# Optimization experiments

Hardware: AMD Instinct MI355X
Metric: run time of the kernel (lower is better)

Reference implementation:

```python
import jax, jax.numpy as jnp
import numpy as np

VOCAB, EMBED, HID = 30000, 256, 128
B, T = 256, 512


def setup_inputs() -> dict:
    key = jax.random.key(0)
    ks = jax.random.split(key, 8)
    s_e = 1.0 / np.sqrt(EMBED)
    s_h = 1.0 / np.sqrt(HID)
    return {
        "tokens": jax.random.randint(ks[0], (B, T), 0, VOCAB, dtype=jnp.int32),
        "emb": jax.random.uniform(ks[1], (VOCAB, EMBED), jnp.float32, -0.05, 0.05),
        "W_fw": jax.random.normal(ks[2], (EMBED, 4 * HID), jnp.float32) * s_e,
        "U_fw": jax.random.normal(ks[3], (HID, 4 * HID), jnp.float32) * s_h,
        "b_fw": jnp.zeros((4 * HID,), jnp.float32),
        "W_bw": jax.random.normal(ks[4], (EMBED, 4 * HID), jnp.float32) * s_e,
        "U_bw": jax.random.normal(ks[5], (HID, 4 * HID), jnp.float32) * s_h,
        "b_bw": jnp.zeros((4 * HID,), jnp.float32),
    }


def _lstm_scan(x, W, U, b):
    # x: [B, T, E]; Keras LSTMCell gate order i, f, g(c), o.
    xW = jnp.einsum("bte,eg->btg", x, W) + b  # precompute input projections

    def step(carry, xw_t):
        h, c = carry
        z = xw_t + h @ U  # [B, 4H]
        i, f, g, o = jnp.split(z, 4, axis=-1)
        c = jax.nn.sigmoid(f) * c + jax.nn.sigmoid(i) * jnp.tanh(g)
        h = jax.nn.sigmoid(o) * jnp.tanh(c)
        return (h, c), h

    h0 = jnp.zeros((x.shape[0], U.shape[0]), x.dtype)
    (h_T, c_T), hs = jax.lax.scan(step, (h0, h0), xW.transpose(1, 0, 2))
    return hs.transpose(1, 0, 2), h_T, c_T  # [B,T,H], [B,H], [B,H]


def reference(tokens, emb, W_fw, U_fw, b_fw, W_bw, U_bw, b_bw):
    x = emb[tokens]  # [B, T, E]; Dropout layers are identity in eval mode
    out_f, hf, cf = _lstm_scan(x, W_fw, U_fw, b_fw)
    out_b_rev, hb, cb = _lstm_scan(x[:, ::-1, :], W_bw, U_bw, b_bw)
    out = jnp.concatenate([out_f, out_b_rev[:, ::-1, :]], axis=-1)  # [B,T,2H]
    return out, hf, cf, hb, cb
```

## Files before the change

### kernel.cpp

```cpp
#include <hip/hip_runtime.h>
#include <hip/hip_bf16.h>
#include <stdint.h>

#define VOCAB 30000
#define EMBED 256
#define HID   128
#define BB    256
#define TT    512
#define G4    512
#define GWH   1024

typedef _Float16 f16x8 __attribute__((ext_vector_type(8)));
typedef _Float16 f16x4 __attribute__((ext_vector_type(4)));
typedef float    f32x4 __attribute__((ext_vector_type(4)));

#define S_IFO (-1.4426950408889634f)
#define S_G   ( 2.8853900817779268f)

__device__ __forceinline__ float fexp2(float x){
#if __has_builtin(__builtin_amdgcn_exp2f)
  return __builtin_amdgcn_exp2f(x);
#else
  return exp2f(x);
#endif
}
__device__ __forceinline__ float frcp(float x){
#if __has_builtin(__builtin_amdgcn_rcpf)
  return __builtin_amdgcn_rcpf(x);
#else
  return 1.0f/x;
#endif
}
__device__ __forceinline__ float sigm_p(float zp){
  return frcp(1.0f + fexp2(zp));
}
__device__ __forceinline__ float tanh_p(float zp){
  return 1.0f - 2.0f*frcp(1.0f + fexp2(zp));
}
__device__ __forceinline__ float tanh_rt(float x){
  return 1.0f - 2.0f*frcp(1.0f + fexp2(S_G*x));
}

__global__ __launch_bounds__(256, 4) void embw_mfma(
    const float* __restrict__ emb,
    const float* __restrict__ Wf, const float* __restrict__ Wb,
    const float* __restrict__ bf, const float* __restrict__ bb,
    _Float16* __restrict__ EW)
{
  __shared__ _Float16 As[64*EMBED];
  const int tid  = threadIdx.x;
  const int l    = tid & 63;
  const int w    = tid >> 6;
  const int r0   = blockIdx.x * 64;
  const int dirc = blockIdx.y >> 3;
  const int u0   = (blockIdx.y & 7) * 16;
  const int nr   = min(64, VOCAB - r0);

  const float4* asrc = (const float4*)(emb + (size_t)r0*EMBED);
  for (int i = tid; i < nr*(EMBED/4); i += 256){
    float4 v = asrc[i];
    const int row = i >> 6;
    const int kc  = (i & 63) * 4;
    const int ks  = kc ^ ((row & 7) << 3);
    _Float16* dst = &As[row*EMBED + ks];
    dst[0]=(_Float16)v.x; dst[1]=(_Float16)v.y;
    dst[2]=(_Float16)v.z; dst[3]=(_Float16)v.w;
  }
  __syncthreads();

  const int cl = w*16 + (l & 15);
  const int ul = cl >> 2;
  const int g  = cl & 3;
  const int cg = g*128 + u0 + ul;
  const float* Wsrc = (dirc ? Wb : Wf) + cg;
  const int kg = (l >> 4) * 8;

  f32x4 acc[4] = {{0,0,0,0},{0,0,0,0},{0,0,0,0},{0,0,0,0}};

  for (int kk = 0; kk < EMBED/32; ++kk){
    const int kb = kk*32 + kg;
    f16x8 bfrag;
    #pragma unroll
    for (int j = 0; j < 8; ++j)
      bfrag[j] = (_Float16)Wsrc[(size_t)(kb + j)*G4];
    #pragma unroll
    for (int m = 0; m < 4; ++m){
      const int row = m*16 + (l & 15);
      const int ks  = kb ^ ((row & 7) << 3);
      f16x8 afrag = *(const f16x8*)&As[row*EMBED + ks];
      acc[m] = __builtin_amdgcn_mfma_f32_16x16x32_f16(afrag, bfrag, acc[m], 0, 0, 0);
    }
  }

  const float bv  = (dirc ? bb : bf)[cg];
  const float gsc = (g == 2) ? S_G : S_IFO;
  const int   co  = dirc*512 + (u0 + ul)*4 + g;
  #pragma unroll
  for (int m = 0; m < 4; ++m){
    #pragma unroll
    for (int r = 0; r < 4; ++r){
      const int vrow = r0 + m*16 + (l >> 4)*4 + r;
      if (vrow < VOCAB)
        EW[(size_t)vrow*GWH + co] = (_Float16)((acc[m][r] + bv) * gsc);
    }
  }
}

__global__ __launch_bounds__(512, 2) void lstm_r10(
    const int*      __restrict__ tokens,
    const _Float16* __restrict__ EW,
    const float*    __restrict__ Ufw, const float* __restrict__ Ubw,
    float* __restrict__ out)
{
  __shared__ _Float16 h_lds[2][320];
  __shared__ int      tok_lds[2*TT];

  const int tid = threadIdx.x;
  const int l   = tid & 63;
  const int w   = tid >> 6;
  const int lr  = l & 15;
  const int hi  = l >> 4;
  const int dir = blockIdx.x & 1;
  const int b0  = (blockIdx.x >> 1) * 2;

  if (tid < 640) ((_Float16*)h_lds)[tid] = (_Float16)0.f;
  for (int i = tid; i < 2*TT; i += 512)
    tok_lds[i] = tokens[(b0 + (i >> 9))*TT + (i & 511)];
  __syncthreads();

  const float* U = dir ? Ubw : Ufw;
  f16x8 ub[4][4];
  #pragma unroll
  for (int kt = 0; kt < 4; ++kt){
    #pragma unroll
    for (int g = 0; g < 4; ++g){
      const int   col = g*128 + w*16 + lr;
      const float gs  = (g == 2) ? S_G : S_IFO;
      f16x8 f;
      #pragma unroll
      for (int j = 0; j < 8; ++j)
        f[j] = (_Float16)(U[(size_t)(kt*32 + hi*8 + j)*G4 + col] * gs);
      ub[kt][g] = f;
    }
  }

  const int  bsel = (l >> 2) & 1;
  const bool act  = (l < 32);
  const int  q    = hi & 1;
  const int  u    = w*16 + lr;

  float creg = 0.f, hfin = 0.f;
  const _Float16* ebase = EW + dir*512 + u*4;

  f32x4 aP[4];
  #pragma unroll
  for (int g = 0; g < 4; ++g) aP[g] = (f32x4){0.f,0.f,0.f,0.f};

  #define AADDR(S) ({ int ss_ = (S); ss_ = ss_ < TT ? ss_ : TT-1;            \
                      const int tt_ = dir ? (TT-1-ss_) : ss_;                \
                      ebase + (size_t)tok_lds[q*TT + tt_]*GWH; })

  f16x4 xwA = *(const f16x4*)AADDR(0);
  f16x4 xwB = *(const f16x4*)AADDR(1);
  const _Float16* adA = AADDR(2);
  const _Float16* adB = AADDR(3);

  #define STEP(XW, AD, SCUR, CUR)                                            \
  {                                                                          \
    const int t_ = dir ? (TT-1-(SCUR)) : (SCUR);                             \
    f16x8 ha[4];                                                             \
    _Pragma("unroll")                                                        \
    for (int kt = 0; kt < 4; ++kt)                                           \
      ha[kt] = *(const f16x8*)&h_lds[CUR][bsel*160 + kt*32 + hi*8];          \
    _Pragma("unroll")                                                        \
    for (int g = 0; g < 4; ++g) aP[g][0] = (float)XW[g];                     \
    XW = *(const f16x4*)AD;                 \
    AD = AADDR((SCUR)+4);                   \
    _Pragma("unroll")                                                        \
    for (int kt = 0; kt < 4; ++kt){                                          \
      _Pragma("unroll")                                                      \
      for (int g = 0; g < 4; ++g)                                            \
        aP[g] = __builtin_amdgcn_mfma_f32_16x16x32_f16(ha[kt], ub[kt][g], aP[g], 0,0,0); \
    }                                                                        \
    if (act){                                                                \
      const float si = sigm_p(aP[0][0]);                                     \
      const float sf = sigm_p(aP[1][0]);                                     \
      const float tg = tanh_p(aP[2][0]);                                     \
      const float so = sigm_p(aP[3][0]);                                     \
      const float cn = sf*creg + si*tg;                                      \
      creg = cn;                                                             \
      const float hh = so*tanh_rt(cn);                                       \
      hfin = hh;                                                             \
      h_lds[(CUR)^1][q*160 + u] = (_Float16)hh;                              \
      out[((size_t)(b0+q)*TT + t_)*(2*HID) + (size_t)dir*HID + u] = hh;      \
    }                                                                        \
    asm volatile("s_waitcnt lgkmcnt(0)" ::: "memory");                       \
    __builtin_amdgcn_s_barrier();                                            \
  }

  for (int s = 0; s < TT; s += 2){
    STEP(xwA, adA, s,     0)
    STEP(xwB, adB, s + 1, 1)
  }
  #undef STEP
  #undef AADDR

  if (act){
    const size_t O1  = (size_t)BB*TT*(2*HID);
    const size_t idx = (size_t)(b0+q)*HID + u;
    if (dir == 0){
      out[O1                    + idx] = hfin;
      out[O1 +   (size_t)BB*HID + idx] = creg;
    } else {
      out[O1 + 2*(size_t)BB*HID + idx] = hfin;
      out[O1 + 3*(size_t)BB*HID + idx] = creg;
    }
  }
}

extern "C" void kernel_launch(void* const* d_in, const int* in_sizes, int n_in,
                              void* d_out, int out_size, void* d_ws, size_t ws_size,
                              hipStream_t stream)
{
  const int*   tokens = (const int*)  d_in[0];
  const float* emb    = (const float*)d_in[1];
  const float* Wf     = (const float*)d_in[2];
  const float* Ufw    = (const float*)d_in[3];
  const float* bf     = (const float*)d_in[4];
  const float* Wb     = (const float*)d_in[5];
  const float* Ubw    = (const float*)d_in[6];
  const float* bb     = (const float*)d_in[7];
  float* out = (float*)d_out;
  _Float16* EW = (_Float16*)d_ws;

  embw_mfma<<<dim3((VOCAB + 63)/64, 16), 256, 0, stream>>>(emb, Wf, Wb, bf, bb, EW);
  lstm_r10<<<BB, 512, 0, stream>>>(tokens, EW, Ufw, Ubw, out);
}
```

Baseline: 370.6 us.

## Split recurrent MFMA chain into two accumulators and read tokens from global

The serial per-step chain of 16 dependent MFMAs is split into two independent accumulator sets (aP over k-tiles 0 and 1, aQ over k-tiles 2 and 3), interleaved and summed before the activations. This shortens the dependent MFMA latency on the recurrence's critical path. The token LDS staging is also removed: active lanes now read token ids straight from global memory one step ahead, and the gate-row gather is predicated on active lanes only. The cost is extra accumulator registers and a small global load per step on the prefetch path.

```diff
diff --git a/kernel.cpp b/kernel.cpp
--- a/kernel.cpp
+++ b/kernel.cpp
@@ -106,14 +106,13 @@
   }
 }
 
-__global__ __launch_bounds__(512, 2) void lstm_r10(
+__global__ __launch_bounds__(512, 2) void lstm_r11(
     const int*      __restrict__ tokens,
     const _Float16* __restrict__ EW,
     const float*    __restrict__ Ufw, const float* __restrict__ Ubw,
     float* __restrict__ out)
 {
   __shared__ _Float16 h_lds[2][320];
-  __shared__ int      tok_lds[2*TT];
 
   const int tid = threadIdx.x;
   const int l   = tid & 63;
@@ -124,8 +123,6 @@
   const int b0  = (blockIdx.x >> 1) * 2;
 
   if (tid < 640) ((_Float16*)h_lds)[tid] = (_Float16)0.f;
-  for (int i = tid; i < 2*TT; i += 512)
-    tok_lds[i] = tokens[(b0 + (i >> 9))*TT + (i & 511)];
   __syncthreads();
 
   const float* U = dir ? Ubw : Ufw;
@@ -151,21 +148,25 @@
 
   float creg = 0.f, hfin = 0.f;
   const _Float16* ebase = EW + dir*512 + u*4;
-
-  f32x4 aP[4];
+  const int* tokq = tokens + (size_t)(b0+q)*TT;
+
+  #define TIDX(S) ({ int ss_ = (S); ss_ = ss_ < TT ? ss_ : TT-1;             \
+                     dir ? (TT-1-ss_) : ss_; })
+
+  f32x4 aP[4], aQ[4];
   #pragma unroll
-  for (int g = 0; g < 4; ++g) aP[g] = (f32x4){0.f,0.f,0.f,0.f};
-
-  #define AADDR(S) ({ int ss_ = (S); ss_ = ss_ < TT ? ss_ : TT-1;            \
-                      const int tt_ = dir ? (TT-1-ss_) : ss_;                \
-                      ebase + (size_t)tok_lds[q*TT + tt_]*GWH; })
-
-  f16x4 xwA = *(const f16x4*)AADDR(0);
-  f16x4 xwB = *(const f16x4*)AADDR(1);
-  const _Float16* adA = AADDR(2);
-  const _Float16* adB = AADDR(3);
-
-  #define STEP(XW, AD, SCUR, CUR)                                            \
+  for (int g = 0; g < 4; ++g){ aP[g]=(f32x4){0,0,0,0}; aQ[g]=(f32x4){0,0,0,0}; }
+
+  int tkA = 0, tkB = 0;
+  f16x4 xwA = {0,0,0,0}, xwB = {0,0,0,0};
+  if (act){
+    xwA = *(const f16x4*)(ebase + (size_t)tokq[TIDX(0)]*GWH);
+    xwB = *(const f16x4*)(ebase + (size_t)tokq[TIDX(1)]*GWH);
+    tkA = tokq[TIDX(2)];
+    tkB = tokq[TIDX(3)];
+  }
+
+  #define STEP(XW, TK, SCUR, CUR)                                            \
   {                                                                          \
     const int t_ = dir ? (TT-1-(SCUR)) : (SCUR);                             \
     f16x8 ha[4];                                                             \
@@ -173,20 +174,29 @@
     for (int kt = 0; kt < 4; ++kt)                                           \
       ha[kt] = *(const f16x8*)&h_lds[CUR][bsel*160 + kt*32 + hi*8];          \
     _Pragma("unroll")                                                        \
-    for (int g = 0; g < 4; ++g) aP[g][0] = (float)XW[g];                     \
-    XW = *(const f16x4*)AD;                 \
-    AD = AADDR((SCUR)+4);                   \
-    _Pragma("unroll")                                                        \
-    for (int kt = 0; kt < 4; ++kt){                                          \
-      _Pragma("unroll")                                                      \
-      for (int g = 0; g < 4; ++g)                                            \
-        aP[g] = __builtin_amdgcn_mfma_f32_16x16x32_f16(ha[kt], ub[kt][g], aP[g], 0,0,0); \
+    for (int g = 0; g < 4; ++g){ aP[g][0] = (float)XW[g]; aQ[g][0] = 0.f; }  \
+    if (act){                                                                \
+      const _Float16* ad_ = ebase + (size_t)TK*GWH;  \
+      XW = *(const f16x4*)ad_;                        \
+      TK = tokq[TIDX((SCUR)+4)];                      \
     }                                                                        \
+    _Pragma("unroll")                                                        \
+    for (int g = 0; g < 4; ++g)                                              \
+      aP[g] = __builtin_amdgcn_mfma_f32_16x16x32_f16(ha[0], ub[0][g], aP[g], 0,0,0); \
+    _Pragma("unroll")                                                        \
+    for (int g = 0; g < 4; ++g)                                              \
+      aQ[g] = __builtin_amdgcn_mfma_f32_16x16x32_f16(ha[2], ub[2][g], aQ[g], 0,0,0); \
+    _Pragma("unroll")                                                        \
+    for (int g = 0; g < 4; ++g)                                              \
+      aP[g] = __builtin_amdgcn_mfma_f32_16x16x32_f16(ha[1], ub[1][g], aP[g], 0,0,0); \
+    _Pragma("unroll")                                                        \
+    for (int g = 0; g < 4; ++g)                                              \
+      aQ[g] = __builtin_amdgcn_mfma_f32_16x16x32_f16(ha[3], ub[3][g], aQ[g], 0,0,0); \
     if (act){                                                                \
-      const float si = sigm_p(aP[0][0]);                                     \
-      const float sf = sigm_p(aP[1][0]);                                     \
-      const float tg = tanh_p(aP[2][0]);                                     \
-      const float so = sigm_p(aP[3][0]);                                     \
+      const float si = sigm_p(aP[0][0] + aQ[0][0]);                          \
+      const float sf = sigm_p(aP[1][0] + aQ[1][0]);                          \
+      const float tg = tanh_p(aP[2][0] + aQ[2][0]);                          \
+      const float so = sigm_p(aP[3][0] + aQ[3][0]);                          \
       const float cn = sf*creg + si*tg;                                      \
       creg = cn;                                                             \
       const float hh = so*tanh_rt(cn);                                       \
@@ -199,11 +209,11 @@
   }
 
   for (int s = 0; s < TT; s += 2){
-    STEP(xwA, adA, s,     0)
-    STEP(xwB, adB, s + 1, 1)
+    STEP(xwA, tkA, s,     0)
+    STEP(xwB, tkB, s + 1, 1)
   }
   #undef STEP
-  #undef AADDR
+  #undef TIDX
 
   if (act){
     const size_t O1  = (size_t)BB*TT*(2*HID);
@@ -234,5 +244,5 @@
   _Float16* EW = (_Float16*)d_ws;
 
   embw_mfma<<<dim3((VOCAB + 63)/64, 16), 256, 0, stream>>>(emb, Wf, Wb, bf, bb, EW);
-  lstm_r10<<<BB, 512, 0, stream>>>(tokens, EW, Ufw, Ubw, out);
-}
+  lstm_r11<<<BB, 512, 0, stream>>>(tokens, EW, Ufw, Ubw, out);
+}
```

Result: slower. 389.5 us (+5.1%).

## Interleave forward and backward LSTM directions in one block per batch row

Applied to the files above, without the earlier changes.

Each block now handles a single batch row and runs both directions, alternating phases so the gate activations of one direction overlap the MFMA recurrence of the other. Before, each block handled two batch rows of a single direction. The aim is to hide the serial latency between the MFMA and the gate math within each timestep. In exchange, register pressure doubles because both directions' U fragments are held in registers, and only 16 lanes per wave do gate work.

```diff
diff --git a/kernel.cpp b/kernel.cpp
--- a/kernel.cpp
+++ b/kernel.cpp
@@ -31,15 +31,9 @@
   return 1.0f/x;
 #endif
 }
-__device__ __forceinline__ float sigm_p(float zp){
-  return frcp(1.0f + fexp2(zp));
-}
-__device__ __forceinline__ float tanh_p(float zp){
-  return 1.0f - 2.0f*frcp(1.0f + fexp2(zp));
-}
-__device__ __forceinline__ float tanh_rt(float x){
-  return 1.0f - 2.0f*frcp(1.0f + fexp2(S_G*x));
-}
+__device__ __forceinline__ float sigm_p(float zp){ return frcp(1.0f + fexp2(zp)); }
+__device__ __forceinline__ float tanh_p(float zp){ return 1.0f - 2.0f*frcp(1.0f + fexp2(zp)); }
+__device__ __forceinline__ float tanh_rt(float x){ return 1.0f - 2.0f*frcp(1.0f + fexp2(S_G*x)); }
 
 __global__ __launch_bounds__(256, 4) void embw_mfma(
     const float* __restrict__ emb,
@@ -106,115 +100,140 @@
   }
 }
 
-__global__ __launch_bounds__(512, 2) void lstm_r10(
+__global__ __launch_bounds__(512, 2) void lstm_dp(
     const int*      __restrict__ tokens,
     const _Float16* __restrict__ EW,
     const float*    __restrict__ Ufw, const float* __restrict__ Ubw,
     float* __restrict__ out)
 {
-  __shared__ _Float16 h_lds[2][320];
-  __shared__ int      tok_lds[2*TT];
+  __shared__ _Float16 h_lds[2][160];
+  __shared__ int      tok_lds[TT];
 
   const int tid = threadIdx.x;
   const int l   = tid & 63;
   const int w   = tid >> 6;
   const int lr  = l & 15;
   const int hi  = l >> 4;
-  const int dir = blockIdx.x & 1;
-  const int b0  = (blockIdx.x >> 1) * 2;
-
-  if (tid < 640) ((_Float16*)h_lds)[tid] = (_Float16)0.f;
-  for (int i = tid; i < 2*TT; i += 512)
-    tok_lds[i] = tokens[(b0 + (i >> 9))*TT + (i & 511)];
+  const int b   = blockIdx.x;
+
+  if (tid < 320) ((_Float16*)h_lds)[tid] = (_Float16)0.f;
+  if (tid < TT)  tok_lds[tid] = tokens[(size_t)b*TT + tid];
   __syncthreads();
 
-  const float* U = dir ? Ubw : Ufw;
-  f16x8 ub[4][4];
+  f16x8 ub[2][4][4];
   #pragma unroll
-  for (int kt = 0; kt < 4; ++kt){
-    #pragma unroll
-    for (int g = 0; g < 4; ++g){
-      const int   col = g*128 + w*16 + lr;
-      const float gs  = (g == 2) ? S_G : S_IFO;
-      f16x8 f;
+  for (int d = 0; d < 2; ++d){
+    const float* U = d ? Ubw : Ufw;
+    #pragma unroll
+    for (int kt = 0; kt < 4; ++kt){
       #pragma unroll
-      for (int j = 0; j < 8; ++j)
-        f[j] = (_Float16)(U[(size_t)(kt*32 + hi*8 + j)*G4 + col] * gs);
-      ub[kt][g] = f;
-    }
-  }
-
-  const int  bsel = (l >> 2) & 1;
-  const bool act  = (l < 32);
-  const int  q    = hi & 1;
-  const int  u    = w*16 + lr;
-
-  float creg = 0.f, hfin = 0.f;
-  const _Float16* ebase = EW + dir*512 + u*4;
-
-  f32x4 aP[4];
+      for (int g = 0; g < 4; ++g){
+        const int   col = g*128 + w*16 + lr;
+        const float gs  = (g == 2) ? S_G : S_IFO;
+        f16x8 f;
+        #pragma unroll
+        for (int j = 0; j < 8; ++j)
+          f[j] = (_Float16)(U[(size_t)(kt*32 + hi*8 + j)*G4 + col] * gs);
+        ub[d][kt][g] = f;
+      }
+    }
+  }
+
+  const bool act = (l < 16);
+  const int  u   = w*16 + lr;
+
+  float cF = 0.f, cB = 0.f, hFv = 0.f, hBv = 0.f;
+  const _Float16* eb0 = EW +       u*4;
+  const _Float16* eb1 = EW + 512 + u*4;
+
+  #define ADDR_F(S) (eb0 + (size_t)tok_lds[(S) < TT ? (S) : TT-1]*GWH)
+  #define ADDR_B(S) (eb1 + (size_t)tok_lds[(S) < TT ? TT-1-(S) : 0]*GWH)
+
+  f32x4 aF[4], aB[4];
   #pragma unroll
-  for (int g = 0; g < 4; ++g) aP[g] = (f32x4){0.f,0.f,0.f,0.f};
-
-  #define AADDR(S) ({ int ss_ = (S); ss_ = ss_ < TT ? ss_ : TT-1;            \
-                      const int tt_ = dir ? (TT-1-ss_) : ss_;                \
-                      ebase + (size_t)tok_lds[q*TT + tt_]*GWH; })
-
-  f16x4 xwA = *(const f16x4*)AADDR(0);
-  f16x4 xwB = *(const f16x4*)AADDR(1);
-  const _Float16* adA = AADDR(2);
-  const _Float16* adB = AADDR(3);
-
-  #define STEP(XW, AD, SCUR, CUR)                                            \
-  {                                                                          \
-    const int t_ = dir ? (TT-1-(SCUR)) : (SCUR);                             \
-    f16x8 ha[4];                                                             \
+  for (int g = 0; g < 4; ++g){ aF[g]=(f32x4){0,0,0,0}; aB[g]=(f32x4){0,0,0,0}; }
+
+  f16x4 xwF = {0,0,0,0}, xwB = {0,0,0,0};
+  const _Float16 *adF = eb0, *adB = eb1;
+  if (act){
+    xwF = *(const f16x4*)ADDR_F(0);
+    xwB = *(const f16x4*)ADDR_B(0);
+    adF = ADDR_F(1);
+    adB = ADDR_B(1);
+    #pragma unroll
+    for (int g = 0; g < 4; ++g){ aF[g][0] = (float)xwF[g]; aB[g][0] = (float)xwB[g]; }
+    xwF = *(const f16x4*)adF;  adF = ADDR_F(2);
+    xwB = *(const f16x4*)adB;  adB = ADDR_B(2);
+  }
+
+  #define MFMA_PH(ACC, D)                                                    \
+  { f16x8 ha[4];                                                             \
     _Pragma("unroll")                                                        \
     for (int kt = 0; kt < 4; ++kt)                                           \
-      ha[kt] = *(const f16x8*)&h_lds[CUR][bsel*160 + kt*32 + hi*8];          \
-    _Pragma("unroll")                                                        \
-    for (int g = 0; g < 4; ++g) aP[g][0] = (float)XW[g];                     \
-    XW = *(const f16x4*)AD;                 \
-    AD = AADDR((SCUR)+4);                   \
+      ha[kt] = *(const f16x8*)&h_lds[D][kt*32 + hi*8];                       \
     _Pragma("unroll")                                                        \
     for (int kt = 0; kt < 4; ++kt){                                          \
       _Pragma("unroll")                                                      \
       for (int g = 0; g < 4; ++g)                                            \
-        aP[g] = __builtin_amdgcn_mfma_f32_16x16x32_f16(ha[kt], ub[kt][g], aP[g], 0,0,0); \
-    }                                                                        \
-    if (act){                                                                \
-      const float si = sigm_p(aP[0][0]);                                     \
-      const float sf = sigm_p(aP[1][0]);                                     \
-      const float tg = tanh_p(aP[2][0]);                                     \
-      const float so = sigm_p(aP[3][0]);                                     \
-      const float cn = sf*creg + si*tg;                                      \
-      creg = cn;                                                             \
-      const float hh = so*tanh_rt(cn);                                       \
-      hfin = hh;                                                             \
-      h_lds[(CUR)^1][q*160 + u] = (_Float16)hh;                              \
-      out[((size_t)(b0+q)*TT + t_)*(2*HID) + (size_t)dir*HID + u] = hh;      \
-    }                                                                        \
-    asm volatile("s_waitcnt lgkmcnt(0)" ::: "memory");                       \
-    __builtin_amdgcn_s_barrier();                                            \
-  }
-
-  for (int s = 0; s < TT; s += 2){
-    STEP(xwA, adA, s,     0)
-    STEP(xwB, adB, s + 1, 1)
-  }
-  #undef STEP
-  #undef AADDR
+        ACC[g] = __builtin_amdgcn_mfma_f32_16x16x32_f16(ha[kt], ub[D][kt][g], ACC[g], 0,0,0); \
+    } }
+
+  #define GATE_PH(ACC, XW, AD, ADDR_M, CREG, HFIN, SNEXT, T_, DIRC)          \
+  if (act){                                                                  \
+    const float si = sigm_p(ACC[0][0]);                                      \
+    const float sf = sigm_p(ACC[1][0]);                                      \
+    const float tg = tanh_p(ACC[2][0]);                                      \
+    const float so = sigm_p(ACC[3][0]);                                      \
+    const float cn = sf*CREG + si*tg;                                        \
+    CREG = cn;                                                               \
+    const float hh = so*tanh_rt(cn);                                         \
+    HFIN = hh;                                                               \
+    h_lds[DIRC][u] = (_Float16)hh;                                           \
+    out[((size_t)b*TT + (T_))*(2*HID) + (size_t)(DIRC)*HID + u] = hh;        \
+    _Pragma("unroll")                                                        \
+    for (int g = 0; g < 4; ++g) ACC[g][0] = (float)XW[g];                    \
+    XW = *(const f16x4*)AD;                                                  \
+    AD = ADDR_M(SNEXT);                                                      \
+  }
+
+  for (int i = 0; i < TT; ++i){
+    if (i > 0){
+      GATE_PH(aB, xwB, adB, ADDR_B, cB, hBv, i+2, (TT-1-(i-1)), 1)
+    }
+    MFMA_PH(aF, 0)
+    asm volatile("s_waitcnt lgkmcnt(0)" ::: "memory");
+    __builtin_amdgcn_s_barrier();
+
+    GATE_PH(aF, xwF, adF, ADDR_F, cF, hFv, i+3, i, 0)
+    MFMA_PH(aB, 1)
+    asm volatile("s_waitcnt lgkmcnt(0)" ::: "memory");
+    __builtin_amdgcn_s_barrier();
+  }
+
+  if (act){
+    const float si = sigm_p(aB[0][0]);
+    const float sf = sigm_p(aB[1][0]);
+    const float tg = tanh_p(aB[2][0]);
+    const float so = sigm_p(aB[3][0]);
+    const float cn = sf*cB + si*tg;
+    cB = cn;
+    const float hh = so*tanh_rt(cn);
+    hBv = hh;
+    out[((size_t)b*TT + 0)*(2*HID) + HID + u] = hh;
+  }
+
+  #undef GATE_PH
+  #undef MFMA_PH
+  #undef ADDR_F
+  #undef ADDR_B
 
   if (act){
     const size_t O1  = (size_t)BB*TT*(2*HID);
-    const size_t idx = (size_t)(b0+q)*HID + u;
-    if (dir == 0){
-      out[O1                    + idx] = hfin;
-      out[O1 +   (size_t)BB*HID + idx] = creg;
-    } else {
-      out[O1 + 2*(size_t)BB*HID + idx] = hfin;
-      out[O1 + 3*(size_t)BB*HID + idx] = creg;
-    }
+    const size_t idx = (size_t)b*HID + u;
+    out[O1                        + idx] = hFv;
+    out[O1 +   (size_t)BB*HID     + idx] = cF;
+    out[O1 + 2*(size_t)BB*HID     + idx] = hBv;
+    out[O1 + 3*(size_t)BB*HID     + idx] = cB;
   }
 }
 
@@ -234,5 +253,5 @@
   _Float16* EW = (_Float16*)d_ws;
 
   embw_mfma<<<dim3((VOCAB + 63)/64, 16), 256, 0, stream>>>(emb, Wf, Wb, bf, bb, EW);
-  lstm_r10<<<BB, 512, 0, stream>>>(tokens, EW, Ufw, Ubw, out);
-}
+  lstm_dp<<<BB, 512, 0, stream>>>(tokens, EW, Ufw, Ubw, out);
+}
```

Result: slower. 574.5 us (+55.0%).

## Process 16 batch rows per LSTM block to fill MFMA rows

Applied to the files above, without the earlier changes.

Each recurrent block now handles 16 batch sequences instead of 2, so all 16 rows of each MFMA tile carry real work and every lane runs the gate activations for 4 rows. The hidden state in LDS becomes a 16x128 tile with an XOR swizzle to avoid bank conflicts. The input projections now enter as the MFMA accumulator seed rather than being written into a zeroed accumulator. The grid shrinks from 256 to 32 blocks, which leaves most compute units idle while each block does 8x the per-step work on a serial time loop.

```diff
diff --git a/kernel.cpp b/kernel.cpp
--- a/kernel.cpp
+++ b/kernel.cpp
@@ -9,6 +9,7 @@
 #define TT    512
 #define G4    512
 #define GWH   1024
+#define BPB   16
 
 typedef _Float16 f16x8 __attribute__((ext_vector_type(8)));
 typedef _Float16 f16x4 __attribute__((ext_vector_type(4)));
@@ -31,15 +32,9 @@
   return 1.0f/x;
 #endif
 }
-__device__ __forceinline__ float sigm_p(float zp){
-  return frcp(1.0f + fexp2(zp));
-}
-__device__ __forceinline__ float tanh_p(float zp){
-  return 1.0f - 2.0f*frcp(1.0f + fexp2(zp));
-}
-__device__ __forceinline__ float tanh_rt(float x){
-  return 1.0f - 2.0f*frcp(1.0f + fexp2(S_G*x));
-}
+__device__ __forceinline__ float sigm_p(float zp){ return frcp(1.0f + fexp2(zp)); }
+__device__ __forceinline__ float tanh_p(float zp){ return 1.0f - 2.0f*frcp(1.0f + fexp2(zp)); }
+__device__ __forceinline__ float tanh_rt(float x){ return 1.0f - 2.0f*frcp(1.0f + fexp2(S_G*x)); }
 
 __global__ __launch_bounds__(256, 4) void embw_mfma(
     const float* __restrict__ emb,
@@ -106,14 +101,14 @@
   }
 }
 
-__global__ __launch_bounds__(512, 2) void lstm_r10(
+__global__ __launch_bounds__(512, 2) void lstm_b16(
     const int*      __restrict__ tokens,
     const _Float16* __restrict__ EW,
     const float*    __restrict__ Ufw, const float* __restrict__ Ubw,
     float* __restrict__ out)
 {
-  __shared__ _Float16 h_lds[2][320];
-  __shared__ int      tok_lds[2*TT];
+  __shared__ _Float16 h_lds[2][16*HID];
+  __shared__ int      tok_lds[BPB*TT];
 
   const int tid = threadIdx.x;
   const int l   = tid & 63;
@@ -121,10 +116,10 @@
   const int lr  = l & 15;
   const int hi  = l >> 4;
   const int dir = blockIdx.x & 1;
-  const int b0  = (blockIdx.x >> 1) * 2;
-
-  if (tid < 640) ((_Float16*)h_lds)[tid] = (_Float16)0.f;
-  for (int i = tid; i < 2*TT; i += 512)
+  const int b0  = (blockIdx.x >> 1) * BPB;
+
+  for (int i = tid; i < 2*16*HID; i += 512) ((_Float16*)h_lds)[i] = (_Float16)0.f;
+  for (int i = tid; i < BPB*TT; i += 512)
     tok_lds[i] = tokens[(b0 + (i >> 9))*TT + (i & 511)];
   __syncthreads();
 
@@ -144,76 +139,108 @@
     }
   }
 
-  const int  bsel = (l >> 2) & 1;
-  const bool act  = (l < 32);
-  const int  q    = hi & 1;
-  const int  u    = w*16 + lr;
-
-  float creg = 0.f, hfin = 0.f;
+  const int u = w*16 + lr;
+  f32x4 creg = {0.f,0.f,0.f,0.f};
+  float hfin[4] = {0.f,0.f,0.f,0.f};
   const _Float16* ebase = EW + dir*512 + u*4;
-
-  f32x4 aP[4];
+  float* outp[4];
   #pragma unroll
-  for (int g = 0; g < 4; ++g) aP[g] = (f32x4){0.f,0.f,0.f,0.f};
-
-  #define AADDR(S) ({ int ss_ = (S); ss_ = ss_ < TT ? ss_ : TT-1;            \
-                      const int tt_ = dir ? (TT-1-ss_) : ss_;                \
-                      ebase + (size_t)tok_lds[q*TT + tt_]*GWH; })
-
-  f16x4 xwA = *(const f16x4*)AADDR(0);
-  f16x4 xwB = *(const f16x4*)AADDR(1);
-  const _Float16* adA = AADDR(2);
-  const _Float16* adB = AADDR(3);
-
-  #define STEP(XW, AD, SCUR, CUR)                                            \
+  for (int r = 0; r < 4; ++r)
+    outp[r] = out + (size_t)(b0 + hi*4 + r)*TT*(2*HID) + (size_t)dir*HID + u;
+
+  #define TIDX(S) ({ int ss_ = (S); ss_ = ss_ < TT ? ss_ : TT-1;             \
+                     dir ? (TT-1-ss_) : ss_; })
+
+  f16x4 ldA[4], ldB[4];
+  const _Float16 *adA[4], *adB[4];
+  {
+    const int t0 = TIDX(0), t1 = TIDX(1), t2 = TIDX(2), t3 = TIDX(3);
+    #pragma unroll
+    for (int r = 0; r < 4; ++r){
+      ldA[r] = *(const f16x4*)(ebase + (size_t)tok_lds[(hi*4+r)*TT + t0]*GWH);
+      ldB[r] = *(const f16x4*)(ebase + (size_t)tok_lds[(hi*4+r)*TT + t1]*GWH);
+      adA[r] = ebase + (size_t)tok_lds[(hi*4+r)*TT + t2]*GWH;
+      adB[r] = ebase + (size_t)tok_lds[(hi*4+r)*TT + t3]*GWH;
+    }
+  }
+
+  #define STEP(LD, AD, SCUR, CUR)                                            \
   {                                                                          \
     const int t_ = dir ? (TT-1-(SCUR)) : (SCUR);                             \
+         \
     f16x8 ha[4];                                                             \
     _Pragma("unroll")                                                        \
-    for (int kt = 0; kt < 4; ++kt)                                           \
-      ha[kt] = *(const f16x8*)&h_lds[CUR][bsel*160 + kt*32 + hi*8];          \
-    _Pragma("unroll")                                                        \
-    for (int g = 0; g < 4; ++g) aP[g][0] = (float)XW[g];                     \
-    XW = *(const f16x4*)AD;                 \
-    AD = AADDR((SCUR)+4);                   \
-    _Pragma("unroll")                                                        \
     for (int kt = 0; kt < 4; ++kt){                                          \
+      const int chunk = (kt*4 + hi) ^ (lr & 7);                              \
+      ha[kt] = *(const f16x8*)&h_lds[CUR][lr*HID + chunk*8];                 \
+    }                                                                        \
+    int tk4[4];                                                              \
+    { const int t4 = TIDX((SCUR)+4);                                         \
+      _Pragma("unroll")                                                      \
+      for (int r = 0; r < 4; ++r) tk4[r] = tok_lds[(hi*4+r)*TT + t4]; }      \
+                                         \
+    f32x4 cin[4];                                                            \
+    _Pragma("unroll")                                                        \
+    for (int g = 0; g < 4; ++g){                                             \
+      _Pragma("unroll")                                                      \
+      for (int r = 0; r < 4; ++r) cin[g][r] = (float)LD[r][g];               \
+    }                                                                        \
+        \
+    _Pragma("unroll")                                                        \
+    for (int r = 0; r < 4; ++r){                                             \
+      LD[r] = *(const f16x4*)AD[r];                                          \
+      AD[r] = ebase + (size_t)tk4[r]*GWH;                                    \
+    }                                                                        \
+                      \
+    f32x4 acc[4];                                                            \
+    _Pragma("unroll")                                                        \
+    for (int g = 0; g < 4; ++g)                                              \
+      acc[g] = __builtin_amdgcn_mfma_f32_16x16x32_f16(ha[0], ub[0][g], cin[g], 0,0,0); \
+    _Pragma("unroll")                                                        \
+    for (int kt = 1; kt < 4; ++kt){                                          \
       _Pragma("unroll")                                                      \
       for (int g = 0; g < 4; ++g)                                            \
-        aP[g] = __builtin_amdgcn_mfma_f32_16x16x32_f16(ha[kt], ub[kt][g], aP[g], 0,0,0); \
-    }                                                                        \
-    if (act){                                                                \
-      const float si = sigm_p(aP[0][0]);                                     \
-      const float sf = sigm_p(aP[1][0]);                                     \
-      const float tg = tanh_p(aP[2][0]);                                     \
-      const float so = sigm_p(aP[3][0]);                                     \
-      const float cn = sf*creg + si*tg;                                      \
-      creg = cn;                                                             \
+        acc[g] = __builtin_amdgcn_mfma_f32_16x16x32_f16(ha[kt], ub[kt][g], acc[g], 0,0,0); \
+    }                                                                        \
+                         \
+    _Pragma("unroll")                                                        \
+    for (int r = 0; r < 4; ++r){                                             \
+      const float si = sigm_p(acc[0][r]);                                    \
+      const float sf = sigm_p(acc[1][r]);                                    \
+      const float tg = tanh_p(acc[2][r]);                                    \
+      const float so = sigm_p(acc[3][r]);                                    \
+      const float cn = sf*creg[r] + si*tg;                                   \
+      creg[r] = cn;                                                          \
       const float hh = so*tanh_rt(cn);                                       \
-      hfin = hh;                                                             \
-      h_lds[(CUR)^1][q*160 + u] = (_Float16)hh;                              \
-      out[((size_t)(b0+q)*TT + t_)*(2*HID) + (size_t)dir*HID + u] = hh;      \
+      hfin[r] = hh;                                                          \
+      const int row  = hi*4 + r;                                             \
+      const int fidx = row*HID + ((((u >> 3) ^ (row & 7)) & 15) << 3) + (u & 7); \
+      h_lds[(CUR)^1][fidx] = (_Float16)hh;                                   \
+      outp[r][(size_t)t_*(2*HID)] = hh;                                      \
     }                                                                        \
     asm volatile("s_waitcnt lgkmcnt(0)" ::: "memory");                       \
     __builtin_amdgcn_s_barrier();                                            \
   }
 
   for (int s = 0; s < TT; s += 2){
-    STEP(xwA, adA, s,     0)
-    STEP(xwB, adB, s + 1, 1)
+    STEP(ldA, adA, s,     0)
+    STEP(ldB, adB, s + 1, 1)
   }
   #undef STEP
-  #undef AADDR
-
-  if (act){
-    const size_t O1  = (size_t)BB*TT*(2*HID);
-    const size_t idx = (size_t)(b0+q)*HID + u;
-    if (dir == 0){
-      out[O1                    + idx] = hfin;
-      out[O1 +   (size_t)BB*HID + idx] = creg;
-    } else {
-      out[O1 + 2*(size_t)BB*HID + idx] = hfin;
-      out[O1 + 3*(size_t)BB*HID + idx] = creg;
+  #undef TIDX
+
+  {
+    const size_t O1 = (size_t)BB*TT*(2*HID);
+    #pragma unroll
+    for (int r = 0; r < 4; ++r){
+      const size_t idx = (size_t)(b0 + hi*4 + r)*HID + u;
+      if (dir == 0){
+        out[O1                    + idx] = hfin[r];
+        out[O1 +   (size_t)BB*HID + idx] = creg[r];
+      } else {
+        out[O1 + 2*(size_t)BB*HID + idx] = hfin[r];
+        out[O1 + 3*(size_t)BB*HID + idx] = creg[r];
+      }
     }
   }
 }
@@ -234,5 +261,5 @@
   _Float16* EW = (_Float16*)d_ws;
 
   embw_mfma<<<dim3((VOCAB + 63)/64, 16), 256, 0, stream>>>(emb, Wf, Wb, bf, bb, EW);
-  lstm_r10<<<BB, 512, 0, stream>>>(tokens, EW, Ufw, Ubw, out);
-}
+  lstm_b16<<<(BB/BPB)*2, 512, 0, stream>>>(tokens, EW, Ufw, Ubw, out);
+}
```

Result: slower. 581.3 us (+56.8%).
